# Kernel tuning notes

Hardware: AMD Instinct MI355X
Metric: run time of the kernel (lower is better)

## Reference

```python
import jax, jax.numpy as jnp
import numpy as np

# Tree config: batch of perfect binary trees in heap layout (root=0, children of i are 2i+1, 2i+2)
D_MODEL = 512
DEPTH = 10                      # number of internal levels
B = 64                          # number of trees in the batch
VOCAB = 32000
N_LEAVES = 2 ** DEPTH           # 1024 leaves per tree
N_NODES = 2 ** (DEPTH + 1) - 1  # 2047 nodes per tree
N_CLASSES = 2                   # binary graph classification


def setup_inputs() -> dict:
    key = jax.random.key(0)
    k_tok, k_emb, k_iou, k_f, k_out = jax.random.split(key, 5)
    d = D_MODEL
    s_in = 1.0 / np.sqrt(2 * d)
    return {
        "tokens": jax.random.randint(k_tok, (B, N_LEAVES), 0, VOCAB, dtype=jnp.int32),
        "embedding": (jax.random.normal(k_emb, (VOCAB, d), jnp.float32) * 0.02),
        "W_iou": jax.random.normal(k_iou, (2 * d, 3 * d), jnp.float32) * s_in,
        "b_iou": jnp.zeros((3 * d,), jnp.float32),
        "W_f": jax.random.normal(k_f, (2 * d, 2 * d), jnp.float32) * s_in,
        "b_f": jnp.zeros((2 * d,), jnp.float32),
        "W_out": jax.random.normal(k_out, (d, N_CLASSES), jnp.float32) * (1.0 / np.sqrt(d)),
    }


def reference(tokens, embedding, W_iou, b_iou, W_f, b_f, W_out):
    # Shared activation / memory buffers over all nodes, as in RecursiveNN.forward.
    d = embedding.shape[1]
    b = tokens.shape[0]
    h = jnp.zeros((b, N_NODES, d), jnp.float32)   # activations
    c = jnp.zeros((b, N_NODES, d), jnp.float32)   # memory (memory_size=1)

    # Leaves: embedding lookup, scattered into the activation buffer.
    leaf_h = embedding[tokens]                    # [B, N_LEAVES, d]
    h = h.at[:, N_LEAVES - 1:].set(leaf_h)

    # Internal nodes by topological level (leaf-adjacent level first, root last).
    for level in range(DEPTH - 1, -1, -1):
        idx = np.arange(2 ** level - 1, 2 ** (level + 1) - 1)  # node group (static)
        left, right = 2 * idx + 1, 2 * idx + 2                 # predecessor indices
        # Gather predecessor activations and memory.
        hl, hr = h[:, left], h[:, right]                       # [B, n, d]
        cl, cr = c[:, left], c[:, right]
        x = jnp.concatenate([hl, hr], axis=-1)                 # [B, n, 2d]
        # Binary TreeLSTM cell (the _apply_function for the 'add' binary op).
        iou = x @ W_iou + b_iou
        i, o, u = jnp.split(iou, 3, axis=-1)
        f = jax.nn.sigmoid(x @ W_f + b_f)
        fl, fr = jnp.split(f, 2, axis=-1)
        c_new = jax.nn.sigmoid(i) * jnp.tanh(u) + fl * cl + fr * cr
        h_new = jax.nn.sigmoid(o) * jnp.tanh(c_new)
        # Scatter back into the shared buffers.
        h = h.at[:, idx].set(h_new)
        c = c.at[:, idx].set(c_new)

    # _compute_output: linear binary-classification head on the root activation.
    return h[:, 0] @ W_out                                     # [B, N_CLASSES]
```

## Files before the change

### kernel.cpp

```cpp
#include <hip/hip_runtime.h>
#include <math.h>

typedef unsigned short u16;
typedef short s16x8 __attribute__((ext_vector_type(8)));
typedef float f32x4 __attribute__((ext_vector_type(4)));

#define NITER 32
#define ARW 72

__device__ __align__(16) u16 g_Bhi[1024 * 2560];
__device__ __align__(16) u16 g_Blo[1024 * 2560];

__device__ __forceinline__ u16 f2bf(float x) {
    unsigned u = __float_as_uint(x);
    u += 0x7fffu + ((u >> 16) & 1u);
    return (u16)(u >> 16);
}
__device__ __forceinline__ float bf2f(u16 h) { return __uint_as_float(((unsigned)h) << 16); }
__device__ __forceinline__ float sigm(float x) { return 1.0f / (1.0f + expf(-x)); }
__device__ __forceinline__ unsigned pk(u16 a, u16 b) { return (unsigned)a | ((unsigned)b << 16); }

__global__ __launch_bounds__(256)
void wsplit_kernel(const float* __restrict__ Wiou, const float* __restrict__ Wf)
{
    __shared__ float tile[32][65];
    const int kb = blockIdx.x;
    const int cb = blockIdx.y;
    const int t  = threadIdx.x;
    const int c0 = cb * 64;

    {
        const int kk  = t >> 3;
        const int cu0 = (t & 7) * 8;
        const int k   = kb * 32 + kk;
#pragma unroll
        for (int u = 0; u < 8; u++) {
            int c = c0 + cu0 + u;
            float v = (c < 1536) ? Wiou[(size_t)k * 1536 + c]
                                 : Wf[(size_t)k * 1024 + (c - 1536)];
            tile[kk][cu0 + u] = v;
        }
    }
    __syncthreads();
    {
        const int jl = t >> 2;
        const int kc = (t & 3) * 8;
        const int g  = c0 >> 9;
        const int j  = (c0 & 511) + jl;
        size_t dst = (((size_t)kb * 5 + g) * 512 + j) * 32 + kc;
        unsigned ph[4], pl[4];
#pragma unroll
        for (int u = 0; u < 4; u++) {
            float v0 = tile[kc + 2 * u][jl];
            float v1 = tile[kc + 2 * u + 1][jl];
            u16 h0 = f2bf(v0), h1 = f2bf(v1);
            u16 l0 = f2bf(v0 - bf2f(h0)), l1 = f2bf(v1 - bf2f(h1));
            ph[u] = pk(h0, h1);
            pl[u] = pk(l0, l1);
        }
        *(uint4*)(g_Bhi + dst) = make_uint4(ph[0], ph[1], ph[2], ph[3]);
        *(uint4*)(g_Blo + dst) = make_uint4(pl[0], pl[1], pl[2], pl[3]);
    }
}

template<bool LEAF>
__global__ __launch_bounds__(256, 2)
void level_mfma(const u16* __restrict__ Hc, const float* __restrict__ Cc,
                const int* __restrict__ tokens, const float* __restrict__ emb,
                const float* __restrict__ b_iou, const float* __restrict__ b_f,
                u16* __restrict__ Hp, float* __restrict__ Cp,
                int np, int lgnp)
{
    __shared__ __align__(16) u16 Ac[2][64 * ARW];

    const int tid = threadIdx.x;
    const int jg  = blockIdx.x;
    const int m0  = blockIdx.y * 64;
    const int j0  = jg * 64;
    const int nc  = np * 2;
    const int M   = np * 64;

    const int w    = tid >> 6;
    const int lane = tid & 63;
    const int il   = lane & 15;
    const int kq   = lane >> 4;
    const int wc   = w;

    f32x4 acc[4][5];
#pragma unroll
    for (int rf = 0; rf < 4; rf++)
#pragma unroll
        for (int g = 0; g < 5; g++) acc[rf][g] = (f32x4)0.0f;

    const int rA = tid >> 2;
    const int qA = tid & 3;
    int mA = m0 + rA; if (mA > M - 1) mA = M - 1;
    const int bA = mA >> lgnp;
    const int pA = mA & (np - 1);

    const u16* arow = nullptr;
    const float *erowL = nullptr, *erowR = nullptr;
    if (LEAF) {
        int tl = tokens[bA * 1024 + 2 * pA];
        int tr = tokens[bA * 1024 + 2 * pA + 1];
        erowL = emb + (size_t)tl * 512;
        erowR = emb + (size_t)tr * 512;
    } else {
        arow = Hc + ((size_t)bA * nc + 2 * pA) * 1024;
    }
    const int daI = rA * ARW + (qA & 1) * 32 + (qA >> 1) * 16;
    const int daL = rA * ARW + qA * 8;

    const u16* bbH = g_Bhi + ((size_t)(j0 + wc * 16 + il)) * 32 + kq * 8;
    const u16* bbL = g_Blo + ((size_t)(j0 + wc * 16 + il)) * 32 + kq * 8;

    uint4  aR0, aR1;
    float4 fR0, fR1;
    s16x8 b0h[5], b0l[5], b1h[5], b1l[5];

#define LOADA(t_)                                                              \
    {                                                                          \
        const int t__ = (t_);                                                  \
        if (LEAF) {                                                            \
            const float* asrc = ((t__ < 16) ? erowL : erowR)                   \
                                + ((32 * t__) & 511) + qA * 8;                 \
            fR0 = *(const float4*)asrc;                                        \
            fR1 = *(const float4*)(asrc + 4);                                  \
        } else {                                                               \
            const u16* asrc = arow + t__ * 64 + qA * 16;                       \
            aR0 = *(const uint4*)asrc;                                         \
            aR1 = *(const uint4*)(asrc + 8);                                   \
        }                                                                      \
    }

#define LOADB(BH, BL, t_)                                                      \
    {                                                                          \
        const size_t tb = (size_t)(t_) * 5 * 16384;                            \
        _Pragma("unroll")                                                      \
        for (int g = 0; g < 5; g++) {                                          \
            BH[g] = *(const s16x8*)(bbH + tb + (size_t)g * 16384);             \
            BL[g] = *(const s16x8*)(bbL + tb + (size_t)g * 16384);             \
        }                                                                      \
    }

#define WRITEA(bf)                                                             \
    {                                                                          \
        const int bf__ = (bf);                                                 \
        if (LEAF) {                                                            \
            float v[8] = {fR0.x, fR0.y, fR0.z, fR0.w, fR1.x, fR1.y, fR1.z, fR1.w}; \
            unsigned ph[4], pl[4];                                             \
            _Pragma("unroll")                                                  \
            for (int i = 0; i < 4; i++) {                                      \
                u16 h0 = f2bf(v[2 * i]), h1 = f2bf(v[2 * i + 1]);              \
                u16 l0 = f2bf(v[2 * i] - bf2f(h0));                            \
                u16 l1 = f2bf(v[2 * i + 1] - bf2f(h1));                        \
                ph[i] = pk(h0, h1);  pl[i] = pk(l0, l1);                       \
            }                                                                  \
            *(uint4*)&Ac[bf__][daL]      = make_uint4(ph[0], ph[1], ph[2], ph[3]); \
            *(uint4*)&Ac[bf__][daL + 32] = make_uint4(pl[0], pl[1], pl[2], pl[3]); \
        } else {                                                               \
            *(uint4*)&Ac[bf__][daI]     = aR0;                                 \
            *(uint4*)&Ac[bf__][daI + 8] = aR1;                                 \
        }                                                                      \
    }

#define COMPUTE(BH, BL, BUF)                                                   \
    {                                                                          \
        _Pragma("unroll")                                                      \
        for (int rf = 0; rf < 4; rf++) {                                       \
            const int ao = (rf * 16 + il) * ARW + kq * 8;                      \
            s16x8 ahv = *(const s16x8*)&Ac[BUF][ao];                           \
            s16x8 alv = *(const s16x8*)&Ac[BUF][ao + 32];                      \
            _Pragma("unroll")                                                  \
            for (int g = 0; g < 5; g++) {                                      \
                acc[rf][g] = __builtin_amdgcn_mfma_f32_16x16x32_bf16(ahv, BH[g], acc[rf][g], 0, 0, 0); \
                acc[rf][g] = __builtin_amdgcn_mfma_f32_16x16x32_bf16(ahv, BL[g], acc[rf][g], 0, 0, 0); \
                acc[rf][g] = __builtin_amdgcn_mfma_f32_16x16x32_bf16(alv, BH[g], acc[rf][g], 0, 0, 0); \
            }                                                                  \
        }                                                                      \
    }

    LOADA(0);
    LOADB(b0h, b0l, 0);
    WRITEA(0);
    __syncthreads();

#pragma unroll 1
    for (int t = 0; t < NITER; t += 2) {
        if (t + 1 < NITER) {
            LOADA(t + 1);
            LOADB(b1h, b1l, t + 1);
        }
        COMPUTE(b0h, b0l, 0);
        if (t + 1 < NITER) {
            WRITEA(1);
            __syncthreads();
        }
        if (t + 2 < NITER) {
            LOADA(t + 2);
            LOADB(b0h, b0l, t + 2);
        }
        COMPUTE(b1h, b1l, 1);
        if (t + 2 < NITER) {
            WRITEA(0);
            __syncthreads();
        }
    }
#undef LOADA
#undef LOADB
#undef WRITEA
#undef COMPUTE

    const int jglob = j0 + wc * 16 + il;
    const float bi  = b_iou[jglob];
    const float bo_ = b_iou[512 + jglob];
    const float bu  = b_iou[1024 + jglob];
    const float bfl = b_f[jglob];
    const float bfr = b_f[512 + jglob];

#pragma unroll
    for (int rf = 0; rf < 4; rf++) {
#pragma unroll
        for (int r = 0; r < 4; r++) {
            const int m = m0 + rf * 16 + kq * 4 + r;
            if (m < M) {
                const int b = m >> lgnp;
                const int p = m & (np - 1);
                float i_ = acc[rf][0][r] + bi;
                float o_ = acc[rf][1][r] + bo_;
                float u_ = acc[rf][2][r] + bu;
                float fl = sigm(acc[rf][3][r] + bfl);
                float fr = sigm(acc[rf][4][r] + bfr);
                float cl = 0.0f, cr_ = 0.0f;
                if (!LEAF) {
                    size_t cb_ = ((size_t)b * nc + 2 * p) * 512 + jglob;
                    cl  = Cc[cb_];
                    cr_ = Cc[cb_ + 512];
                }
                float cn = sigm(i_) * tanhf(u_) + fl * cl + fr * cr_;
                float hn = sigm(o_) * tanhf(cn);
                size_t prow = (size_t)b * np + p;
                u16 hh = f2bf(hn);
                u16 hlo = f2bf(hn - bf2f(hh));
                Hp[prow * 1024 + (size_t)(jg * 4 + wc) * 32 + il]      = hh;
                Hp[prow * 1024 + (size_t)(jg * 4 + wc) * 32 + 16 + il] = hlo;
                Cp[prow * 512 + jglob] = cn;
            }
        }
    }
}

__global__ __launch_bounds__(256)
void out_kernel(const u16* __restrict__ Hroot, const float* __restrict__ W_out,
                float* __restrict__ out)
{
    const int b = blockIdx.x;
    const int tid = threadIdx.x;
    float s0 = 0.f, s1 = 0.f;
    for (int d = tid; d < 512; d += 256) {
        const u16* row = Hroot + (size_t)b * 1024 + (d >> 4) * 32 + (d & 15);
        float h = bf2f(row[0]) + bf2f(row[16]);
        s0 = fmaf(h, W_out[d * 2 + 0], s0);
        s1 = fmaf(h, W_out[d * 2 + 1], s1);
    }
#pragma unroll
    for (int off = 32; off > 0; off >>= 1) {
        s0 += __shfl_down(s0, off, 64);
        s1 += __shfl_down(s1, off, 64);
    }
    __shared__ float red[2][4];
    const int wave = tid >> 6;
    if ((tid & 63) == 0) { red[0][wave] = s0; red[1][wave] = s1; }
    __syncthreads();
    if (tid == 0) {
        float t0 = 0.f, t1 = 0.f;
#pragma unroll
        for (int wv = 0; wv < 4; wv++) { t0 += red[0][wv]; t1 += red[1][wv]; }
        out[b * 2 + 0] = t0;
        out[b * 2 + 1] = t1;
    }
}

extern "C" void kernel_launch(void* const* d_in, const int* in_sizes, int n_in,
                              void* d_out, int out_size, void* d_ws, size_t ws_size,
                              hipStream_t stream)
{
    const int*   tokens = (const int*)  d_in[0];
    const float* emb    = (const float*)d_in[1];
    const float* W_iou  = (const float*)d_in[2];
    const float* b_iou  = (const float*)d_in[3];
    const float* W_f    = (const float*)d_in[4];
    const float* b_f    = (const float*)d_in[5];
    const float* W_out  = (const float*)d_in[6];
    float* out = (float*)d_out;

    u16*   H0 = (u16*)d_ws;
    float* C0 = (float*)(H0 + (size_t)512 * 64 * 1024);
    u16*   H1 = (u16*)(C0 + (size_t)512 * 64 * 512);
    float* C1 = (float*)(H1 + (size_t)256 * 64 * 1024);

    wsplit_kernel<<<dim3(32, 40), 256, 0, stream>>>(W_iou, W_f);

    level_mfma<true><<<dim3(8, 512), 256, 0, stream>>>(
        nullptr, nullptr, tokens, emb, b_iou, b_f, H0, C0, 512, 9);

    u16* Hc = H0;  float* Cc = C0;
    u16* Hp = H1;  float* Cp = C1;
    for (int L = 8; L >= 0; L--) {
        const int np = 1 << L;
        level_mfma<false><<<dim3(8, np), 256, 0, stream>>>(
            Hc, Cc, nullptr, nullptr, b_iou, b_f, Hp, Cp, np, L);
        u16* tH = Hc; Hc = Hp; Hp = tH;
        float* tC = Cc; Cc = Cp; Cp = tC;
    }

    out_kernel<<<64, 256, 0, stream>>>(Hc, W_out, out);
}
```

Before: 1.286 ms.

## Pre-gather leaf embeddings to split-bf16 buffer and load A directly into registers

A new pass gathers leaf embeddings and splits them into hi/lo bf16 once, writing them to a global buffer in the same layout as internal-node activations. The leaf-level kernel then no longer converts embeddings inside the MMA loop. For large levels, a new kernel reads A fragments straight from global memory into registers, which removes the LDS staging and the __syncthreads calls. Small levels keep the LDS-based kernel. The trade-off is 128MB of extra global traffic and storage for the leaf buffer, plus A-fragment reads that are less coalesced.

```diff
diff --git a/kernel.cpp b/kernel.cpp
--- a/kernel.cpp
+++ b/kernel.cpp
@@ -10,6 +10,7 @@
 
 __device__ __align__(16) u16 g_Bhi[1024 * 2560];
 __device__ __align__(16) u16 g_Blo[1024 * 2560];
+__device__ __align__(16) u16 g_Aleaf[(size_t)64 * 1024 * 1024];
 
 __device__ __forceinline__ u16 f2bf(float x) {
     unsigned u = __float_as_uint(x);
@@ -63,13 +64,169 @@
     }
 }
 
+__global__ __launch_bounds__(256)
+void leafgather_kernel(const int* __restrict__ tokens, const float* __restrict__ emb)
+{
+    const int gidx = blockIdx.x * 256 + threadIdx.x;
+    const int row  = gidx >> 5;
+    const int c    = gidx & 31;
+    const int tok  = tokens[row];
+    const float* src = emb + (size_t)tok * 512 + c * 16;
+    u16* dst = g_Aleaf + (size_t)row * 1024 + c * 32;
+
+    float4 f0 = *(const float4*)(src);
+    float4 f1 = *(const float4*)(src + 4);
+    float4 f2 = *(const float4*)(src + 8);
+    float4 f3 = *(const float4*)(src + 12);
+    float v[16] = {f0.x,f0.y,f0.z,f0.w, f1.x,f1.y,f1.z,f1.w,
+                   f2.x,f2.y,f2.z,f2.w, f3.x,f3.y,f3.z,f3.w};
+    unsigned ph[8], pl[8];
+#pragma unroll
+    for (int i = 0; i < 8; i++) {
+        u16 h0 = f2bf(v[2*i]),   h1 = f2bf(v[2*i+1]);
+        u16 l0 = f2bf(v[2*i]   - bf2f(h0));
+        u16 l1 = f2bf(v[2*i+1] - bf2f(h1));
+        ph[i] = pk(h0, h1);
+        pl[i] = pk(l0, l1);
+    }
+    *(uint4*)(dst)      = make_uint4(ph[0], ph[1], ph[2], ph[3]);
+    *(uint4*)(dst + 8)  = make_uint4(ph[4], ph[5], ph[6], ph[7]);
+    *(uint4*)(dst + 16) = make_uint4(pl[0], pl[1], pl[2], pl[3]);
+    *(uint4*)(dst + 24) = make_uint4(pl[4], pl[5], pl[6], pl[7]);
+}
+
 template<bool LEAF>
 __global__ __launch_bounds__(256, 2)
-void level_mfma(const u16* __restrict__ Hc, const float* __restrict__ Cc,
-                const int* __restrict__ tokens, const float* __restrict__ emb,
-                const float* __restrict__ b_iou, const float* __restrict__ b_f,
-                u16* __restrict__ Hp, float* __restrict__ Cp,
-                int np, int lgnp)
+void level_big(const u16* __restrict__ Hcin, const float* __restrict__ Cc,
+               const float* __restrict__ b_iou, const float* __restrict__ b_f,
+               u16* __restrict__ Hp, float* __restrict__ Cp,
+               int np, int lgnp)
+{
+    const u16* Hc = LEAF ? g_Aleaf : Hcin;
+
+    const int tid = threadIdx.x;
+    const int jg  = blockIdx.x;
+    const int m0  = blockIdx.y * 64;
+    const int j0  = jg * 64;
+    const int nc  = np * 2;
+
+    const int w    = tid >> 6;
+    const int lane = tid & 63;
+    const int il   = lane & 15;
+    const int kq   = lane >> 4;
+    const int wc   = w;
+
+    f32x4 acc[4][5];
+#pragma unroll
+    for (int rf = 0; rf < 4; rf++)
+#pragma unroll
+        for (int g = 0; g < 5; g++) acc[rf][g] = (f32x4)0.0f;
+
+    const int bA  = m0 >> lgnp;
+    const int pA0 = m0 & (np - 1);
+    const u16* Abase = Hc + ((size_t)bA * nc + 2 * pA0) * 1024;
+    int voffA[4];
+#pragma unroll
+    for (int rf = 0; rf < 4; rf++)
+        voffA[rf] = (rf * 16 + il) * 4096 + (kq >> 1) * 64 + (kq & 1) * 16;
+
+    const u16* bbH = g_Bhi + ((size_t)(j0 + wc * 16 + il)) * 32 + kq * 8;
+    const u16* bbL = g_Blo + ((size_t)(j0 + wc * 16 + il)) * 32 + kq * 8;
+
+    s16x8 a0[8], a1[8];
+    s16x8 b0h[5], b0l[5], b1h[5], b1l[5];
+
+#define LOADA(AR, t_)                                                          \
+    {                                                                          \
+        _Pragma("unroll")                                                      \
+        for (int rf = 0; rf < 4; rf++) {                                       \
+            const u16* p = (const u16*)((const char*)Abase + (voffA[rf] + (t_) * 128)); \
+            AR[2 * rf]     = *(const s16x8*)p;                                 \
+            AR[2 * rf + 1] = *(const s16x8*)(p + 16);                          \
+        }                                                                      \
+    }
+
+#define LOADB(BH, BL, t_)                                                      \
+    {                                                                          \
+        const size_t tb = (size_t)(t_) * 5 * 16384;                            \
+        _Pragma("unroll")                                                      \
+        for (int g = 0; g < 5; g++) {                                          \
+            BH[g] = *(const s16x8*)(bbH + tb + (size_t)g * 16384);             \
+            BL[g] = *(const s16x8*)(bbL + tb + (size_t)g * 16384);             \
+        }                                                                      \
+    }
+
+#define COMPUTE(AR, BH, BL)                                                    \
+    {                                                                          \
+        _Pragma("unroll")                                                      \
+        for (int rf = 0; rf < 4; rf++) {                                       \
+            s16x8 ahv = AR[2 * rf];                                            \
+            s16x8 alv = AR[2 * rf + 1];                                        \
+            _Pragma("unroll")                                                  \
+            for (int g = 0; g < 5; g++) {                                      \
+                acc[rf][g] = __builtin_amdgcn_mfma_f32_16x16x32_bf16(ahv, BH[g], acc[rf][g], 0, 0, 0); \
+                acc[rf][g] = __builtin_amdgcn_mfma_f32_16x16x32_bf16(ahv, BL[g], acc[rf][g], 0, 0, 0); \
+                acc[rf][g] = __builtin_amdgcn_mfma_f32_16x16x32_bf16(alv, BH[g], acc[rf][g], 0, 0, 0); \
+            }                                                                  \
+        }                                                                      \
+    }
+
+    LOADA(a0, 0);
+    LOADB(b0h, b0l, 0);
+
+#pragma unroll 1
+    for (int t = 0; t < NITER; t += 2) {
+        if (t + 1 < NITER) { LOADA(a1, t + 1); LOADB(b1h, b1l, t + 1); }
+        COMPUTE(a0, b0h, b0l);
+        if (t + 2 < NITER) { LOADA(a0, t + 2); LOADB(b0h, b0l, t + 2); }
+        COMPUTE(a1, b1h, b1l);
+    }
+#undef LOADA
+#undef LOADB
+#undef COMPUTE
+
+    const int jglob = j0 + wc * 16 + il;
+    const float bi  = b_iou[jglob];
+    const float bo_ = b_iou[512 + jglob];
+    const float bu  = b_iou[1024 + jglob];
+    const float bfl = b_f[jglob];
+    const float bfr = b_f[512 + jglob];
+
+#pragma unroll
+    for (int rf = 0; rf < 4; rf++) {
+#pragma unroll
+        for (int r = 0; r < 4; r++) {
+            const int m  = m0 + rf * 16 + kq * 4 + r;
+            const int b  = m >> lgnp;
+            const int p  = m & (np - 1);
+            float i_ = acc[rf][0][r] + bi;
+            float o_ = acc[rf][1][r] + bo_;
+            float u_ = acc[rf][2][r] + bu;
+            float fl = sigm(acc[rf][3][r] + bfl);
+            float fr = sigm(acc[rf][4][r] + bfr);
+            float cl = 0.0f, cr_ = 0.0f;
+            if (!LEAF) {
+                size_t cb_ = ((size_t)b * nc + 2 * p) * 512 + jglob;
+                cl  = Cc[cb_];
+                cr_ = Cc[cb_ + 512];
+            }
+            float cn = sigm(i_) * tanhf(u_) + fl * cl + fr * cr_;
+            float hn = sigm(o_) * tanhf(cn);
+            size_t prow = (size_t)b * np + p;
+            u16 hh  = f2bf(hn);
+            u16 hlo = f2bf(hn - bf2f(hh));
+            Hp[prow * 1024 + (size_t)(jg * 4 + wc) * 32 + il]      = hh;
+            Hp[prow * 1024 + (size_t)(jg * 4 + wc) * 32 + 16 + il] = hlo;
+            Cp[prow * 512 + jglob] = cn;
+        }
+    }
+}
+
+__global__ __launch_bounds__(256, 2)
+void level_small(const u16* __restrict__ Hc, const float* __restrict__ Cc,
+                 const float* __restrict__ b_iou, const float* __restrict__ b_f,
+                 u16* __restrict__ Hp, float* __restrict__ Cp,
+                 int np, int lgnp)
 {
     __shared__ __align__(16) u16 Ac[2][64 * ARW];
 
@@ -97,42 +254,21 @@
     int mA = m0 + rA; if (mA > M - 1) mA = M - 1;
     const int bA = mA >> lgnp;
     const int pA = mA & (np - 1);
-
-    const u16* arow = nullptr;
-    const float *erowL = nullptr, *erowR = nullptr;
-    if (LEAF) {
-        int tl = tokens[bA * 1024 + 2 * pA];
-        int tr = tokens[bA * 1024 + 2 * pA + 1];
-        erowL = emb + (size_t)tl * 512;
-        erowR = emb + (size_t)tr * 512;
-    } else {
-        arow = Hc + ((size_t)bA * nc + 2 * pA) * 1024;
-    }
+    const u16* arow = Hc + ((size_t)bA * nc + 2 * pA) * 1024;
     const int daI = rA * ARW + (qA & 1) * 32 + (qA >> 1) * 16;
-    const int daL = rA * ARW + qA * 8;
 
     const u16* bbH = g_Bhi + ((size_t)(j0 + wc * 16 + il)) * 32 + kq * 8;
     const u16* bbL = g_Blo + ((size_t)(j0 + wc * 16 + il)) * 32 + kq * 8;
 
     uint4  aR0, aR1;
-    float4 fR0, fR1;
     s16x8 b0h[5], b0l[5], b1h[5], b1l[5];
 
 #define LOADA(t_)                                                              \
     {                                                                          \
-        const int t__ = (t_);                                                  \
-        if (LEAF) {                                                            \
-            const float* asrc = ((t__ < 16) ? erowL : erowR)                   \
-                                + ((32 * t__) & 511) + qA * 8;                 \
-            fR0 = *(const float4*)asrc;                                        \
-            fR1 = *(const float4*)(asrc + 4);                                  \
-        } else {                                                               \
-            const u16* asrc = arow + t__ * 64 + qA * 16;                       \
-            aR0 = *(const uint4*)asrc;                                         \
-            aR1 = *(const uint4*)(asrc + 8);                                   \
-        }                                                                      \
-    }
-
+        const u16* asrc = arow + (t_) * 64 + qA * 16;                          \
+        aR0 = *(const uint4*)asrc;                                             \
+        aR1 = *(const uint4*)(asrc + 8);                                       \
+    }
 #define LOADB(BH, BL, t_)                                                      \
     {                                                                          \
         const size_t tb = (size_t)(t_) * 5 * 16384;                            \
@@ -142,28 +278,11 @@
             BL[g] = *(const s16x8*)(bbL + tb + (size_t)g * 16384);             \
         }                                                                      \
     }
-
 #define WRITEA(bf)                                                             \
     {                                                                          \
-        const int bf__ = (bf);                                                 \
-        if (LEAF) {                                                            \
-            float v[8] = {fR0.x, fR0.y, fR0.z, fR0.w, fR1.x, fR1.y, fR1.z, fR1.w}; \
-            unsigned ph[4], pl[4];                                             \
-            _Pragma("unroll")                                                  \
-            for (int i = 0; i < 4; i++) {                                      \
-                u16 h0 = f2bf(v[2 * i]), h1 = f2bf(v[2 * i + 1]);              \
-                u16 l0 = f2bf(v[2 * i] - bf2f(h0));                            \
-                u16 l1 = f2bf(v[2 * i + 1] - bf2f(h1));                        \
-                ph[i] = pk(h0, h1);  pl[i] = pk(l0, l1);                       \
-            }                                                                  \
-            *(uint4*)&Ac[bf__][daL]      = make_uint4(ph[0], ph[1], ph[2], ph[3]); \
-            *(uint4*)&Ac[bf__][daL + 32] = make_uint4(pl[0], pl[1], pl[2], pl[3]); \
-        } else {                                                               \
-            *(uint4*)&Ac[bf__][daI]     = aR0;                                 \
-            *(uint4*)&Ac[bf__][daI + 8] = aR1;                                 \
-        }                                                                      \
-    }
-
+        *(uint4*)&Ac[bf][daI]     = aR0;                                       \
+        *(uint4*)&Ac[bf][daI + 8] = aR1;                                       \
+    }
 #define COMPUTE(BH, BL, BUF)                                                   \
     {                                                                          \
         _Pragma("unroll")                                                      \
@@ -187,24 +306,12 @@
 
 #pragma unroll 1
     for (int t = 0; t < NITER; t += 2) {
-        if (t + 1 < NITER) {
-            LOADA(t + 1);
-            LOADB(b1h, b1l, t + 1);
-        }
+        if (t + 1 < NITER) { LOADA(t + 1); LOADB(b1h, b1l, t + 1); }
         COMPUTE(b0h, b0l, 0);
-        if (t + 1 < NITER) {
-            WRITEA(1);
-            __syncthreads();
-        }
-        if (t + 2 < NITER) {
-            LOADA(t + 2);
-            LOADB(b0h, b0l, t + 2);
-        }
+        if (t + 1 < NITER) { WRITEA(1); __syncthreads(); }
+        if (t + 2 < NITER) { LOADA(t + 2); LOADB(b0h, b0l, t + 2); }
         COMPUTE(b1h, b1l, 1);
-        if (t + 2 < NITER) {
-            WRITEA(0);
-            __syncthreads();
-        }
+        if (t + 2 < NITER) { WRITEA(0); __syncthreads(); }
     }
 #undef LOADA
 #undef LOADB
@@ -231,16 +338,13 @@
                 float u_ = acc[rf][2][r] + bu;
                 float fl = sigm(acc[rf][3][r] + bfl);
                 float fr = sigm(acc[rf][4][r] + bfr);
-                float cl = 0.0f, cr_ = 0.0f;
-                if (!LEAF) {
-                    size_t cb_ = ((size_t)b * nc + 2 * p) * 512 + jglob;
-                    cl  = Cc[cb_];
-                    cr_ = Cc[cb_ + 512];
-                }
+                size_t cb_ = ((size_t)b * nc + 2 * p) * 512 + jglob;
+                float cl  = Cc[cb_];
+                float cr_ = Cc[cb_ + 512];
                 float cn = sigm(i_) * tanhf(u_) + fl * cl + fr * cr_;
                 float hn = sigm(o_) * tanhf(cn);
                 size_t prow = (size_t)b * np + p;
-                u16 hh = f2bf(hn);
+                u16 hh  = f2bf(hn);
                 u16 hlo = f2bf(hn - bf2f(hh));
                 Hp[prow * 1024 + (size_t)(jg * 4 + wc) * 32 + il]      = hh;
                 Hp[prow * 1024 + (size_t)(jg * 4 + wc) * 32 + 16 + il] = hlo;
@@ -300,16 +404,22 @@
     float* C1 = (float*)(H1 + (size_t)256 * 64 * 1024);
 
     wsplit_kernel<<<dim3(32, 40), 256, 0, stream>>>(W_iou, W_f);
-
-    level_mfma<true><<<dim3(8, 512), 256, 0, stream>>>(
-        nullptr, nullptr, tokens, emb, b_iou, b_f, H0, C0, 512, 9);
+    leafgather_kernel<<<8192, 256, 0, stream>>>(tokens, emb);
+
+    level_big<true><<<dim3(8, 512), 256, 0, stream>>>(
+        nullptr, nullptr, b_iou, b_f, H0, C0, 512, 9);
 
     u16* Hc = H0;  float* Cc = C0;
     u16* Hp = H1;  float* Cp = C1;
     for (int L = 8; L >= 0; L--) {
         const int np = 1 << L;
-        level_mfma<false><<<dim3(8, np), 256, 0, stream>>>(
-            Hc, Cc, nullptr, nullptr, b_iou, b_f, Hp, Cp, np, L);
+        if (np >= 64) {
+            level_big<false><<<dim3(8, np), 256, 0, stream>>>(
+                Hc, Cc, b_iou, b_f, Hp, Cp, np, L);
+        } else {
+            level_small<<<dim3(8, np), 256, 0, stream>>>(
+                Hc, Cc, b_iou, b_f, Hp, Cp, np, L);
+        }
         u16* tH = Hc; Hc = Hp; Hp = tH;
         float* tC = Cc; Cc = Cp; Cp = tC;
     }
```

Result: slower. 1.797 ms (+39.8%).
